# Kernel tuning notes

Measured on AMD Instinct MI355X. Metric: run time of the kernel, lower is better.

Reference implementation:

```python
import itertools
import jax, jax.numpy as jnp
import numpy as np

ORDER = 3  # MaskDE(order=3) -> DescartesExtension orders 2..3
D = 80
B = 8192


def setup_inputs() -> dict:
    key = jax.random.key(0)
    kx, km = jax.random.split(key)
    x = jax.random.normal(kx, (B, D), dtype=jnp.float32)
    mask = jax.random.randint(km, (D,), 0, 2).astype(jnp.bool_)
    return {"x": x, "mask": mask}


def _comb_indices(m: int, order: int) -> np.ndarray:
    # combinations with replacement of range(m), shape (n_comb, order)
    return np.array(list(itertools.combinations_with_replacement(range(m), order)), dtype=np.int32)


def reference(x, mask):
    # mask is a concrete bool vector: masked_select == static gather
    idx = np.flatnonzero(np.asarray(mask))  # (m,)
    m = idx.size
    xm = x[:, idx]  # (B, m)
    parts = [xm]
    for order in range(2, ORDER + 1):
        combs = _comb_indices(m, order)           # (C, order)
        # gather-multiply-reduce: prod of each feature combination
        parts.append(jnp.prod(xm[:, combs], axis=-1))  # (B, C)
    return jnp.concatenate(parts, axis=-1)
```

## Files before the change

### kernel.cpp

```cpp
#include <hip/hip_runtime.h>
#include <stdint.h>

#define DMAX 80

__global__ void maskde_setup(const void* __restrict__ mask_raw, int m,
                             int* __restrict__ idx_out,
                             uint32_t* __restrict__ table, int P) {
    int tid = blockIdx.x * blockDim.x + threadIdx.x;
    if (tid == 0) {
        const uint8_t* b8  = (const uint8_t*)mask_raw;
        const int*     b32 = (const int*)mask_raw;
        const float*   bf  = (const float*)mask_raw;
        int cnt = 0; bool ok = true;
        for (int i = 0; i < DMAX; ++i) { uint8_t v = b8[i]; if (v > 1) ok = false; cnt += (v != 0); }
        int mode;
        if (ok && cnt == m) {
            mode = 0;
        } else {
            cnt = 0; ok = true;
            for (int i = 0; i < DMAX; ++i) { int v = b32[i]; if (v != 0 && v != 1) ok = false; cnt += (v != 0); }
            mode = (ok && cnt == m) ? 1 : 2;
        }
        int k = 0;
        for (int i = 0; i < DMAX && k < m; ++i) {
            bool on = (mode == 0) ? (b8[i] != 0)
                    : (mode == 1) ? (b32[i] != 0)
                                  : (bf[i] != 0.0f);
            if (on) idx_out[k++] = i;
        }
    }

    int stride = gridDim.x * blockDim.x;
    for (int p = tid; p < P; p += stride) {
        int rem = p, i = 0;
        while (rem >= m - i) { rem -= (m - i); ++i; }
        int j = i + rem;

        if (p < m) {
            table[p] = (uint32_t)p | ((uint32_t)m << 8) | ((uint32_t)m << 16);
        }
        table[m + p] = (uint32_t)i | ((uint32_t)j << 8) | ((uint32_t)m << 16);

        int mi = m - i;
        long long Si  = ((long long)m * (m + 1) * (m + 2)
                       - (long long)mi * (mi + 1) * (mi + 2)) / 6;
        int Rij = ((m - i) + (m - j + 1)) * (j - i) / 2;
        uint32_t* t3 = table + m + P + Si + Rij;
        uint32_t packed_ij = (uint32_t)i | ((uint32_t)j << 8);
        for (int k3 = j; k3 < m; ++k3) {
            t3[k3 - j] = packed_ij | ((uint32_t)k3 << 16);
        }
    }
}

__global__ __launch_bounds__(256) void
maskde_expand(const float* __restrict__ x, const int* __restrict__ idx,
              const uint32_t* __restrict__ table, float* __restrict__ out,
              int m, int T) {
    __shared__ float xls[DMAX + 1];
    const int row = blockIdx.x;
    const int tid = threadIdx.x;

    if (tid <= m) {
        xls[tid] = (tid < m) ? x[row * DMAX + idx[tid]] : 1.0f;
    }
    __syncthreads();

    float* orow = out + (size_t)row * (size_t)T;

    uintptr_t addr = (uintptr_t)orow;
    int k0 = (int)(((16 - (addr & 15)) & 15) >> 2);
    if (k0 > T) k0 = T;
    if (tid < k0) {
        uint32_t e = table[tid];
        orow[tid] = xls[e & 0xFF] * xls[(e >> 8) & 0xFF] * xls[(e >> 16) & 0xFF];
    }

    const int nv = (T - k0) >> 2;
    const uint32_t* tb = table + k0;
    float4* ov = (float4*)(orow + k0);
    for (int v = tid; v < nv; v += 256) {
        uint32_t e0 = tb[4 * v + 0];
        uint32_t e1 = tb[4 * v + 1];
        uint32_t e2 = tb[4 * v + 2];
        uint32_t e3 = tb[4 * v + 3];
        float4 r;
        r.x = xls[e0 & 0xFF] * xls[(e0 >> 8) & 0xFF] * xls[(e0 >> 16) & 0xFF];
        r.y = xls[e1 & 0xFF] * xls[(e1 >> 8) & 0xFF] * xls[(e1 >> 16) & 0xFF];
        r.z = xls[e2 & 0xFF] * xls[(e2 >> 8) & 0xFF] * xls[(e2 >> 16) & 0xFF];
        r.w = xls[e3 & 0xFF] * xls[(e3 >> 8) & 0xFF] * xls[(e3 >> 16) & 0xFF];
        ov[v] = r;
    }

    int tstart = k0 + 4 * nv;
    int c = tstart + tid;
    if (c < T) {
        uint32_t e = table[c];
        orow[c] = xls[e & 0xFF] * xls[(e >> 8) & 0xFF] * xls[(e >> 16) & 0xFF];
    }
}

extern "C" void kernel_launch(void* const* d_in, const int* in_sizes, int n_in,
                              void* d_out, int out_size, void* d_ws, size_t ws_size,
                              hipStream_t stream) {
    const float* x    = (const float*)d_in[0];
    const void*  mask = d_in[1];
    float*       out  = (float*)d_out;

    int rows = in_sizes[0] / DMAX;
    if (rows <= 0 || out_size <= 0) return;
    long long T = (long long)out_size / rows;

    int m = -1;
    for (int mm = 0; mm <= DMAX; ++mm) {
        long long t = (long long)mm
                    + (long long)mm * (mm + 1) / 2
                    + (long long)mm * (mm + 1) * (mm + 2) / 6;
        if (t == T) { m = mm; break; }
    }
    if (m <= 0) return;

    int* idx        = (int*)d_ws;
    uint32_t* table = (uint32_t*)d_ws + 128;
    int P = m * (m + 1) / 2;

    int sblocks = (P + 255) / 256;
    if (sblocks < 1) sblocks = 1;
    maskde_setup<<<sblocks, 256, 0, stream>>>(mask, m, idx, table, P);
    maskde_expand<<<rows, 256, 0, stream>>>(x, idx, table, out, m, (int)T);
}
```

Measured before the change: 137.2 us.

## Process eight rows per block with shared pair products and nontemporal stores

Each block now handles eight rows, spaced four rows apart, instead of one. It first computes all pairwise products x_i*x_j per row into shared memory. Each order-3 output is then one shared pair product times one feature, looked up through a reorganized column table that is read once and reused across the eight rows. Output writes use nontemporal vector stores to avoid cache pollution. This cuts table traffic and multiplications per output, at the cost of a larger shared-memory footprint and fewer blocks in the grid.

```diff
diff --git a/kernel.cpp b/kernel.cpp
--- a/kernel.cpp
+++ b/kernel.cpp
@@ -2,10 +2,15 @@
 #include <stdint.h>
 
 #define DMAX 80
+#define RPB  8
+#define BLK  256
+
+typedef float f32x4 __attribute__((ext_vector_type(4)));
 
 __global__ void maskde_setup(const void* __restrict__ mask_raw, int m,
                              int* __restrict__ idx_out,
-                             uint32_t* __restrict__ table, int P) {
+                             uint32_t* __restrict__ pairtab,
+                             uint32_t* __restrict__ coltab, int P) {
     int tid = blockIdx.x * blockDim.x + threadIdx.x;
     if (tid == 0) {
         const uint8_t* b8  = (const uint8_t*)mask_raw;
@@ -36,67 +41,109 @@
         while (rem >= m - i) { rem -= (m - i); ++i; }
         int j = i + rem;
 
-        if (p < m) {
-            table[p] = (uint32_t)p | ((uint32_t)m << 8) | ((uint32_t)m << 16);
-        }
-        table[m + p] = (uint32_t)i | ((uint32_t)j << 8) | ((uint32_t)m << 16);
+        pairtab[p] = (uint32_t)i | ((uint32_t)j << 8);
+
+        if (p < m)
+            coltab[p] = (uint32_t)P | ((uint32_t)p << 16);
+        coltab[m + p] = (uint32_t)p | ((uint32_t)m << 16);
 
         int mi = m - i;
         long long Si  = ((long long)m * (m + 1) * (m + 2)
                        - (long long)mi * (mi + 1) * (mi + 2)) / 6;
         int Rij = ((m - i) + (m - j + 1)) * (j - i) / 2;
-        uint32_t* t3 = table + m + P + Si + Rij;
-        uint32_t packed_ij = (uint32_t)i | ((uint32_t)j << 8);
-        for (int k3 = j; k3 < m; ++k3) {
-            t3[k3 - j] = packed_ij | ((uint32_t)k3 << 16);
-        }
+        uint32_t* t3 = coltab + m + P + Si + Rij;
+        for (int k3 = j; k3 < m; ++k3)
+            t3[k3 - j] = (uint32_t)p | ((uint32_t)k3 << 16);
     }
 }
 
-__global__ __launch_bounds__(256) void
+__global__ __launch_bounds__(BLK) void
 maskde_expand(const float* __restrict__ x, const int* __restrict__ idx,
-              const uint32_t* __restrict__ table, float* __restrict__ out,
-              int m, int T) {
-    __shared__ float xls[DMAX + 1];
-    const int row = blockIdx.x;
-    const int tid = threadIdx.x;
+              const uint32_t* __restrict__ pairtab,
+              const uint32_t* __restrict__ coltab,
+              float* __restrict__ out,
+              int m, int T, int P, int rows) {
+    extern __shared__ float smem[];
+    const int XSTR  = m + 1;
+    const int PPSTR = P + 1;
+    float* xls = smem;
+    float* pps = smem + RPB * XSTR;
 
-    if (tid <= m) {
-        xls[tid] = (tid < m) ? x[row * DMAX + idx[tid]] : 1.0f;
+    const int cls  = blockIdx.x & 3;
+    const int bi   = blockIdx.x >> 2;
+    const int row0 = cls + 4 * (bi * RPB);
+    const int tid  = threadIdx.x;
+
+    for (int q = tid; q < RPB * XSTR; q += BLK) {
+        int r = q / XSTR, k = q - r * XSTR;
+        int rr = row0 + 4 * r;
+        float v = 1.0f;
+        if (k < m && rr < rows) v = x[rr * DMAX + idx[k]];
+        xls[q] = v;
     }
     __syncthreads();
 
-    float* orow = out + (size_t)row * (size_t)T;
+    for (int r = 0; r < RPB; ++r) {
+        const float* xr = xls + r * XSTR;
+        float*       pr = pps + r * PPSTR;
+        for (int p = tid; p <= P; p += BLK) {
+            float v = 1.0f;
+            if (p < P) {
+                uint32_t ij = pairtab[p];
+                v = xr[ij & 0xFF] * xr[(ij >> 8) & 0xFF];
+            }
+            pr[p] = v;
+        }
+    }
+    __syncthreads();
 
-    uintptr_t addr = (uintptr_t)orow;
-    int k0 = (int)(((16 - (addr & 15)) & 15) >> 2);
+    float* ob[RPB];
+#pragma unroll
+    for (int r = 0; r < RPB; ++r)
+        ob[r] = out + (size_t)(row0 + 4 * r) * (size_t)T;
+
+    uintptr_t a0 = (uintptr_t)ob[0];
+    int k0 = (int)(((16 - (a0 & 15)) & 15) >> 2);
     if (k0 > T) k0 = T;
-    if (tid < k0) {
-        uint32_t e = table[tid];
-        orow[tid] = xls[e & 0xFF] * xls[(e >> 8) & 0xFF] * xls[(e >> 16) & 0xFF];
+    const int nv     = (T - k0) >> 2;
+    const int tstart = k0 + 4 * nv;
+    const int tcnt   = T - tstart;
+    const int scnt   = k0 + tcnt;
+
+    if (scnt > 0) {
+        for (int q = tid; q < RPB * scnt; q += BLK) {
+            int r = q / scnt, w = q - r * scnt;
+            int c = (w < k0) ? w : (tstart + (w - k0));
+            int rr = row0 + 4 * r;
+            if (rr < rows) {
+                uint32_t e = coltab[c];
+                ob[r][c] = pps[r * PPSTR + (int)(e & 0xFFFFu)]
+                         * xls[r * XSTR  + (int)(e >> 16)];
+            }
+        }
     }
 
-    const int nv = (T - k0) >> 2;
-    const uint32_t* tb = table + k0;
-    float4* ov = (float4*)(orow + k0);
-    for (int v = tid; v < nv; v += 256) {
-        uint32_t e0 = tb[4 * v + 0];
-        uint32_t e1 = tb[4 * v + 1];
-        uint32_t e2 = tb[4 * v + 2];
-        uint32_t e3 = tb[4 * v + 3];
-        float4 r;
-        r.x = xls[e0 & 0xFF] * xls[(e0 >> 8) & 0xFF] * xls[(e0 >> 16) & 0xFF];
-        r.y = xls[e1 & 0xFF] * xls[(e1 >> 8) & 0xFF] * xls[(e1 >> 16) & 0xFF];
-        r.z = xls[e2 & 0xFF] * xls[(e2 >> 8) & 0xFF] * xls[(e2 >> 16) & 0xFF];
-        r.w = xls[e3 & 0xFF] * xls[(e3 >> 8) & 0xFF] * xls[(e3 >> 16) & 0xFF];
-        ov[v] = r;
-    }
-
-    int tstart = k0 + 4 * nv;
-    int c = tstart + tid;
-    if (c < T) {
-        uint32_t e = table[c];
-        orow[c] = xls[e & 0xFF] * xls[(e >> 8) & 0xFF] * xls[(e >> 16) & 0xFF];
+    for (int v = tid; v < nv; v += BLK) {
+        const uint32_t* tb = coltab + k0 + 4 * v;
+        uint32_t e0 = tb[0], e1 = tb[1], e2 = tb[2], e3 = tb[3];
+        int p0 = e0 & 0xFFFF, q0 = e0 >> 16;
+        int p1 = e1 & 0xFFFF, q1 = e1 >> 16;
+        int p2 = e2 & 0xFFFF, q2 = e2 >> 16;
+        int p3 = e3 & 0xFFFF, q3 = e3 >> 16;
+#pragma unroll
+        for (int r = 0; r < RPB; ++r) {
+            int rr = row0 + 4 * r;
+            if (rr < rows) {
+                const float* xr = xls + r * XSTR;
+                const float* pr = pps + r * PPSTR;
+                f32x4 o;
+                o.x = pr[p0] * xr[q0];
+                o.y = pr[p1] * xr[q1];
+                o.z = pr[p2] * xr[q2];
+                o.w = pr[p3] * xr[q3];
+                __builtin_nontemporal_store(o, (f32x4*)(ob[r] + k0 + 4 * v));
+            }
+        }
     }
 }
 
@@ -120,12 +167,20 @@
     }
     if (m <= 0) return;
 
-    int* idx        = (int*)d_ws;
-    uint32_t* table = (uint32_t*)d_ws + 128;
     int P = m * (m + 1) / 2;
+
+    int*      idx     = (int*)d_ws;
+    uint32_t* pairtab = (uint32_t*)d_ws + 128;
+    uint32_t* coltab  = pairtab + ((P + 31) & ~31);
 
     int sblocks = (P + 255) / 256;
     if (sblocks < 1) sblocks = 1;
-    maskde_setup<<<sblocks, 256, 0, stream>>>(mask, m, idx, table, P);
-    maskde_expand<<<rows, 256, 0, stream>>>(x, idx, table, out, m, (int)T);
+    maskde_setup<<<sblocks, 256, 0, stream>>>(mask, m, idx, pairtab, coltab, P);
+
+    int rpc    = (rows + 3) / 4;
+    int bpc    = (rpc + RPB - 1) / RPB;
+    int blocks = 4 * bpc;
+    size_t shmem = (size_t)(RPB * (m + 1) + RPB * (P + 1)) * sizeof(float);
+    maskde_expand<<<blocks, BLK, shmem, stream>>>(x, idx, pairtab, coltab, out,
+                                                  m, (int)T, P, rows);
 }
```

Result: slower. 175.4 us (+27.8%).

## Reuse per-row pairwise products in LDS and vectorize index table loads

Applied to the files above, without the earlier changes.

Each row block first computes all pairwise products x_i*x_j into dynamic shared memory. Every output element then becomes one pair product times one single feature, which cuts LDS reads and multiplies per element from three to two. The index table is packed as 16-bit pair index plus feature index. It is replicated in four shifted copies by an extra setup kernel, so the main loop can use aligned uint4 table loads whatever the output row's alignment offset. The cost is an extra kernel launch, a per-row pair-product prepass with an added barrier, and more shared memory per block.

```diff
diff --git a/kernel.cpp b/kernel.cpp
--- a/kernel.cpp
+++ b/kernel.cpp
@@ -2,10 +2,14 @@
 #include <stdint.h>
 
 #define DMAX 80
+#define BLK  256
+
+typedef float f32x4 __attribute__((ext_vector_type(4)));
 
 __global__ void maskde_setup(const void* __restrict__ mask_raw, int m,
                              int* __restrict__ idx_out,
-                             uint32_t* __restrict__ table, int P) {
+                             uint32_t* __restrict__ pairtab,
+                             uint32_t* __restrict__ coltab, int P) {
     int tid = blockIdx.x * blockDim.x + threadIdx.x;
     if (tid == 0) {
         const uint8_t* b8  = (const uint8_t*)mask_raw;
@@ -36,67 +40,88 @@
         while (rem >= m - i) { rem -= (m - i); ++i; }
         int j = i + rem;
 
-        if (p < m) {
-            table[p] = (uint32_t)p | ((uint32_t)m << 8) | ((uint32_t)m << 16);
-        }
-        table[m + p] = (uint32_t)i | ((uint32_t)j << 8) | ((uint32_t)m << 16);
+        pairtab[p] = (uint32_t)i | ((uint32_t)j << 8);
+
+        if (p < m)
+            coltab[p] = (uint32_t)P | ((uint32_t)p << 16);
+        coltab[m + p] = (uint32_t)p | ((uint32_t)m << 16);
 
         int mi = m - i;
         long long Si  = ((long long)m * (m + 1) * (m + 2)
                        - (long long)mi * (mi + 1) * (mi + 2)) / 6;
         int Rij = ((m - i) + (m - j + 1)) * (j - i) / 2;
-        uint32_t* t3 = table + m + P + Si + Rij;
-        uint32_t packed_ij = (uint32_t)i | ((uint32_t)j << 8);
-        for (int k3 = j; k3 < m; ++k3) {
-            t3[k3 - j] = packed_ij | ((uint32_t)k3 << 16);
-        }
+        uint32_t* t3 = coltab + m + P + Si + Rij;
+        for (int k3 = j; k3 < m; ++k3)
+            t3[k3 - j] = (uint32_t)p | ((uint32_t)k3 << 16);
     }
 }
 
-__global__ __launch_bounds__(256) void
+__global__ void maskde_copies(uint32_t* __restrict__ coltab, int tpad, int T,
+                              int m, int P) {
+    int q = blockIdx.x * blockDim.x + threadIdx.x;
+    int total = 3 * tpad;
+    uint32_t sentinel = (uint32_t)P | ((uint32_t)m << 16);
+    for (; q < total; q += gridDim.x * blockDim.x) {
+        int s   = 1 + q / tpad;
+        int off = q - (s - 1) * tpad;
+        uint32_t v = (off + s < T) ? coltab[off + s] : sentinel;
+        coltab[s * tpad + off] = v;
+    }
+}
+
+__global__ __launch_bounds__(BLK) void
 maskde_expand(const float* __restrict__ x, const int* __restrict__ idx,
-              const uint32_t* __restrict__ table, float* __restrict__ out,
-              int m, int T) {
+              const uint32_t* __restrict__ pairtab,
+              const uint32_t* __restrict__ coltab, int tpad,
+              float* __restrict__ out, int m, int T, int P) {
     __shared__ float xls[DMAX + 1];
+    extern __shared__ float pps[];
+
     const int row = blockIdx.x;
     const int tid = threadIdx.x;
 
-    if (tid <= m) {
+    if (tid <= m)
         xls[tid] = (tid < m) ? x[row * DMAX + idx[tid]] : 1.0f;
+    __syncthreads();
+
+    for (int p = tid; p <= P; p += BLK) {
+        float v = 1.0f;
+        if (p < P) {
+            uint32_t ij = pairtab[p];
+            v = xls[ij & 0xFF] * xls[(ij >> 8) & 0xFF];
+        }
+        pps[p] = v;
     }
     __syncthreads();
 
     float* orow = out + (size_t)row * (size_t)T;
+    uintptr_t a0 = (uintptr_t)orow;
+    int k0 = (int)(((16 - (a0 & 15)) & 15) >> 2);
+    if (k0 > T) k0 = T;
 
-    uintptr_t addr = (uintptr_t)orow;
-    int k0 = (int)(((16 - (addr & 15)) & 15) >> 2);
-    if (k0 > T) k0 = T;
     if (tid < k0) {
-        uint32_t e = table[tid];
-        orow[tid] = xls[e & 0xFF] * xls[(e >> 8) & 0xFF] * xls[(e >> 16) & 0xFF];
+        uint32_t e = coltab[tid];
+        orow[tid] = pps[e & 0xFFFF] * xls[e >> 16];
     }
 
     const int nv = (T - k0) >> 2;
-    const uint32_t* tb = table + k0;
-    float4* ov = (float4*)(orow + k0);
-    for (int v = tid; v < nv; v += 256) {
-        uint32_t e0 = tb[4 * v + 0];
-        uint32_t e1 = tb[4 * v + 1];
-        uint32_t e2 = tb[4 * v + 2];
-        uint32_t e3 = tb[4 * v + 3];
-        float4 r;
-        r.x = xls[e0 & 0xFF] * xls[(e0 >> 8) & 0xFF] * xls[(e0 >> 16) & 0xFF];
-        r.y = xls[e1 & 0xFF] * xls[(e1 >> 8) & 0xFF] * xls[(e1 >> 16) & 0xFF];
-        r.z = xls[e2 & 0xFF] * xls[(e2 >> 8) & 0xFF] * xls[(e2 >> 16) & 0xFF];
-        r.w = xls[e3 & 0xFF] * xls[(e3 >> 8) & 0xFF] * xls[(e3 >> 16) & 0xFF];
-        ov[v] = r;
+    const uint4* tbv = (const uint4*)(coltab + (size_t)k0 * (size_t)tpad);
+    float* ovbase = orow + k0;
+
+    for (int v = tid; v < nv; v += BLK) {
+        uint4 e = tbv[v];
+        f32x4 o;
+        o.x = pps[e.x & 0xFFFF] * xls[e.x >> 16];
+        o.y = pps[e.y & 0xFFFF] * xls[e.y >> 16];
+        o.z = pps[e.z & 0xFFFF] * xls[e.z >> 16];
+        o.w = pps[e.w & 0xFFFF] * xls[e.w >> 16];
+        *(f32x4*)(ovbase + 4 * v) = o;
     }
 
-    int tstart = k0 + 4 * nv;
-    int c = tstart + tid;
+    int c = k0 + 4 * nv + tid;
     if (c < T) {
-        uint32_t e = table[c];
-        orow[c] = xls[e & 0xFF] * xls[(e >> 8) & 0xFF] * xls[(e >> 16) & 0xFF];
+        uint32_t e = coltab[c];
+        orow[c] = pps[e & 0xFFFF] * xls[e >> 16];
     }
 }
 
@@ -120,12 +145,21 @@
     }
     if (m <= 0) return;
 
-    int* idx        = (int*)d_ws;
-    uint32_t* table = (uint32_t*)d_ws + 128;
-    int P = m * (m + 1) / 2;
+    int P    = m * (m + 1) / 2;
+    int tpad = (int)((T + 3) & ~3LL);
+
+    int*      idx     = (int*)d_ws;
+    uint32_t* pairtab = (uint32_t*)((char*)d_ws + 1024);
+    uint32_t* coltab  = (uint32_t*)((char*)d_ws + 32768);
 
     int sblocks = (P + 255) / 256;
     if (sblocks < 1) sblocks = 1;
-    maskde_setup<<<sblocks, 256, 0, stream>>>(mask, m, idx, table, P);
-    maskde_expand<<<rows, 256, 0, stream>>>(x, idx, table, out, m, (int)T);
+    maskde_setup<<<sblocks, 256, 0, stream>>>(mask, m, idx, pairtab, coltab, P);
+
+    int cblocks = (3 * tpad + 255) / 256;
+    maskde_copies<<<cblocks, 256, 0, stream>>>(coltab, tpad, (int)T, m, P);
+
+    size_t shmem = (size_t)(P + 1) * sizeof(float);
+    maskde_expand<<<rows, BLK, shmem, stream>>>(x, idx, pairtab, coltab, tpad,
+                                                out, m, (int)T, P);
 }
```

Result: no change. 135.1 us (-1.6%).

## Flatten output into fixed element chunks with precomputed pair products and shifted tables

Applied to the files above, without the earlier changes.

Output is now split into fixed 4096-element chunks instead of one block per row, so every block writes aligned float4 stores over a flat index space. A block may straddle two rows, so it stages both rows' selected features. The block first computes all pairwise products into shared memory, which cuts each order-3 term to a single multiply. Four shifted copies of the column table keep uint4 table loads aligned for any row offset. A separate xsel kernel gathers the masked features up front. This adds a third launch and extra workspace in exchange for better store alignment and less per-element arithmetic.

```diff
diff --git a/kernel.cpp b/kernel.cpp
--- a/kernel.cpp
+++ b/kernel.cpp
@@ -2,11 +2,19 @@
 #include <stdint.h>
 
 #define DMAX 80
+#define BLK  256
+#define XW   96
+#define EPB  4096
+
+typedef float f32x4 __attribute__((ext_vector_type(4)));
 
 __global__ void maskde_setup(const void* __restrict__ mask_raw, int m,
                              int* __restrict__ idx_out,
-                             uint32_t* __restrict__ table, int P) {
+                             uint16_t* __restrict__ pair16,
+                             uint32_t* __restrict__ coltab,
+                             int tpad, int T, int P) {
     int tid = blockIdx.x * blockDim.x + threadIdx.x;
+
     if (tid == 0) {
         const uint8_t* b8  = (const uint8_t*)mask_raw;
         const int*     b32 = (const int*)mask_raw;
@@ -36,67 +44,112 @@
         while (rem >= m - i) { rem -= (m - i); ++i; }
         int j = i + rem;
 
-        if (p < m) {
-            table[p] = (uint32_t)p | ((uint32_t)m << 8) | ((uint32_t)m << 16);
-        }
-        table[m + p] = (uint32_t)i | ((uint32_t)j << 8) | ((uint32_t)m << 16);
+        pair16[p] = (uint16_t)(i | (j << 8));
+
+        #define WR4(c, v) do {                                              \
+            int _c = (c); uint32_t _v = (v);                                \
+            coltab[_c] = _v;                                                \
+            if (_c >= 1) coltab[tpad     + _c - 1] = _v;                    \
+            if (_c >= 2) coltab[2 * tpad + _c - 2] = _v;                    \
+            if (_c >= 3) coltab[3 * tpad + _c - 3] = _v;                    \
+        } while (0)
+
+        if (p < m)
+            WR4(p, (uint32_t)P | ((uint32_t)p << 16));
+        WR4(m + p, (uint32_t)p | ((uint32_t)m << 16));
 
         int mi = m - i;
         long long Si  = ((long long)m * (m + 1) * (m + 2)
                        - (long long)mi * (mi + 1) * (mi + 2)) / 6;
         int Rij = ((m - i) + (m - j + 1)) * (j - i) / 2;
-        uint32_t* t3 = table + m + P + Si + Rij;
-        uint32_t packed_ij = (uint32_t)i | ((uint32_t)j << 8);
-        for (int k3 = j; k3 < m; ++k3) {
-            t3[k3 - j] = packed_ij | ((uint32_t)k3 << 16);
-        }
-    }
-}
-
-__global__ __launch_bounds__(256) void
-maskde_expand(const float* __restrict__ x, const int* __restrict__ idx,
-              const uint32_t* __restrict__ table, float* __restrict__ out,
-              int m, int T) {
-    __shared__ float xls[DMAX + 1];
-    const int row = blockIdx.x;
+        int base = m + P + (int)Si + Rij;
+        for (int k3 = j; k3 < m; ++k3)
+            WR4(base + (k3 - j), (uint32_t)p | ((uint32_t)k3 << 16));
+        #undef WR4
+    }
+}
+
+__global__ void maskde_xsel(const float* __restrict__ x,
+                            const int* __restrict__ idx,
+                            float* __restrict__ xsel, int m, int rows) {
+    int g = blockIdx.x * BLK + threadIdx.x;
+    int total = rows * XW;
+    for (; g < total; g += gridDim.x * BLK) {
+        int row = g / XW, k = g - row * XW;
+        xsel[g] = (k < m) ? x[row * DMAX + idx[k]] : 1.0f;
+    }
+}
+
+__global__ __launch_bounds__(BLK) void
+maskde_expand(const float* __restrict__ xsel,
+              const uint16_t* __restrict__ pair16,
+              const uint32_t* __restrict__ coltab, int tpad,
+              float* __restrict__ out, int m, int T, int P,
+              int rows, int total) {
+    extern __shared__ float sm[];
+    float* xls0 = sm;
+    float* xls1 = sm + XW;
+    float* pps0 = sm + 2 * XW;
+    float* pps1 = pps0 + (P + 1);
+
     const int tid = threadIdx.x;
-
-    if (tid <= m) {
-        xls[tid] = (tid < m) ? x[row * DMAX + idx[tid]] : 1.0f;
+    const int e0  = blockIdx.x * EPB;
+    const int r0  = e0 / T;
+    const int r0start = r0 * T;
+    const bool has1 = (r0 + 1 < rows);
+
+    if (tid < XW) {
+        xls0[tid] = xsel[r0 * XW + tid];
+    } else if (tid >= 128 && tid < 128 + XW) {
+        int k = tid - 128;
+        xls1[k] = has1 ? xsel[(r0 + 1) * XW + k] : 1.0f;
     }
     __syncthreads();
 
-    float* orow = out + (size_t)row * (size_t)T;
-
-    uintptr_t addr = (uintptr_t)orow;
-    int k0 = (int)(((16 - (addr & 15)) & 15) >> 2);
-    if (k0 > T) k0 = T;
-    if (tid < k0) {
-        uint32_t e = table[tid];
-        orow[tid] = xls[e & 0xFF] * xls[(e >> 8) & 0xFF] * xls[(e >> 16) & 0xFF];
-    }
-
-    const int nv = (T - k0) >> 2;
-    const uint32_t* tb = table + k0;
-    float4* ov = (float4*)(orow + k0);
-    for (int v = tid; v < nv; v += 256) {
-        uint32_t e0 = tb[4 * v + 0];
-        uint32_t e1 = tb[4 * v + 1];
-        uint32_t e2 = tb[4 * v + 2];
-        uint32_t e3 = tb[4 * v + 3];
-        float4 r;
-        r.x = xls[e0 & 0xFF] * xls[(e0 >> 8) & 0xFF] * xls[(e0 >> 16) & 0xFF];
-        r.y = xls[e1 & 0xFF] * xls[(e1 >> 8) & 0xFF] * xls[(e1 >> 16) & 0xFF];
-        r.z = xls[e2 & 0xFF] * xls[(e2 >> 8) & 0xFF] * xls[(e2 >> 16) & 0xFF];
-        r.w = xls[e3 & 0xFF] * xls[(e3 >> 8) & 0xFF] * xls[(e3 >> 16) & 0xFF];
-        ov[v] = r;
-    }
-
-    int tstart = k0 + 4 * nv;
-    int c = tstart + tid;
-    if (c < T) {
-        uint32_t e = table[c];
-        orow[c] = xls[e & 0xFF] * xls[(e >> 8) & 0xFF] * xls[(e >> 16) & 0xFF];
+    for (int p = tid; p <= P; p += BLK) {
+        float v0 = 1.0f, v1 = 1.0f;
+        if (p < P) {
+            uint32_t ij = pair16[p];
+            int i = ij & 0xFF, j = (ij >> 8) & 0xFF;
+            v0 = xls0[i] * xls0[j];
+            v1 = xls1[i] * xls1[j];
+        }
+        pps0[p] = v0;
+        pps1[p] = v1;
+    }
+    __syncthreads();
+
+#pragma unroll
+    for (int it = 0; it < EPB / (4 * BLK); ++it) {
+        int ee = e0 + (tid << 2) + it * (4 * BLK);
+        if (ee >= total) break;
+        int c = ee - r0start;
+        const float* pS = pps0;
+        const float* xS = xls0;
+        if (c >= T) { c -= T; pS = pps1; xS = xls1; }
+
+        if (c <= T - 4 && ee + 3 < total) {
+            int s = c & 3;
+            const uint4* tp = (const uint4*)(coltab + (size_t)s * tpad + (c - s));
+            uint4 t = *tp;
+            f32x4 o;
+            o.x = pS[t.x & 0xFFFF] * xS[t.x >> 16];
+            o.y = pS[t.y & 0xFFFF] * xS[t.y >> 16];
+            o.z = pS[t.z & 0xFFFF] * xS[t.z >> 16];
+            o.w = pS[t.w & 0xFFFF] * xS[t.w >> 16];
+            *(f32x4*)(out + ee) = o;
+        } else {
+            for (int u = 0; u < 4; ++u) {
+                int e2 = ee + u;
+                if (e2 >= total) break;
+                int c2 = e2 - r0start;
+                const float* p2 = pps0;
+                const float* x2 = xls0;
+                if (c2 >= T) { c2 -= T; p2 = pps1; x2 = xls1; }
+                uint32_t en = coltab[c2];
+                out[e2] = p2[en & 0xFFFF] * x2[en >> 16];
+            }
+        }
     }
 }
 
@@ -109,23 +162,39 @@
 
     int rows = in_sizes[0] / DMAX;
     if (rows <= 0 || out_size <= 0) return;
-    long long T = (long long)out_size / rows;
+    long long Tll = (long long)out_size / rows;
 
     int m = -1;
     for (int mm = 0; mm <= DMAX; ++mm) {
         long long t = (long long)mm
                     + (long long)mm * (mm + 1) / 2
                     + (long long)mm * (mm + 1) * (mm + 2) / 6;
-        if (t == T) { m = mm; break; }
+        if (t == Tll) { m = mm; break; }
     }
     if (m <= 0) return;
 
-    int* idx        = (int*)d_ws;
-    uint32_t* table = (uint32_t*)d_ws + 128;
-    int P = m * (m + 1) / 2;
+    int T    = (int)Tll;
+    int P    = m * (m + 1) / 2;
+    int tpad = (T + 3) & ~3;
+    int total = rows * T;
+
+    int*      idx    = (int*)d_ws;
+    uint16_t* pair16 = (uint16_t*)((char*)d_ws + 1024);
+    uint32_t* coltab = (uint32_t*)((char*)d_ws + 32768);
+    float*    xsel   = (float*)((char*)d_ws + 32768
+                                + (size_t)4 * tpad * 4 + 256);
 
     int sblocks = (P + 255) / 256;
     if (sblocks < 1) sblocks = 1;
-    maskde_setup<<<sblocks, 256, 0, stream>>>(mask, m, idx, table, P);
-    maskde_expand<<<rows, 256, 0, stream>>>(x, idx, table, out, m, (int)T);
-}
+    maskde_setup<<<sblocks, 256, 0, stream>>>(mask, m, idx, pair16, coltab,
+                                              tpad, T, P);
+
+    int xblocks = (rows * XW + BLK - 1) / BLK;
+    if (xblocks > 2048) xblocks = 2048;
+    maskde_xsel<<<xblocks, BLK, 0, stream>>>(x, idx, xsel, m, rows);
+
+    int nb = (total + EPB - 1) / EPB;
+    size_t shmem = (size_t)(2 * XW + 2 * (P + 1)) * sizeof(float);
+    maskde_expand<<<nb, BLK, shmem, stream>>>(xsel, pair16, coltab, tpad,
+                                              out, m, T, P, rows, total);
+}
```

Measured after the change: 127.6 us. 1.08x faster.
